# Optimization experiments

Hardware: AMD Instinct MI355X
Metric: run time of the kernel (lower is better)

## Reference

```python
import jax, jax.numpy as jnp
import numpy as np

N_NODES = 20000
N_EDGES = 240000
IN_DIM = 20
SH_DIM = 16  # (lmax+1)^2 with lmax=3
DENOM = 1.0
EPS = 1e-12


def spherical_harmonics_lmax3(v):
    """Real spherical harmonics l=0..3 on unit vectors v: [E,3] -> [E,16]."""
    x, y, z = v[:, 0], v[:, 1], v[:, 2]
    x2, y2, z2 = x * x, y * y, z * z
    sh = [
        jnp.full_like(x, 0.28209479177387814),            # l=0
        0.4886025119029199 * y,                            # l=1, m=-1
        0.4886025119029199 * z,                            # l=1, m=0
        0.4886025119029199 * x,                            # l=1, m=1
        1.0925484305920792 * x * y,                        # l=2, m=-2
        1.0925484305920792 * y * z,                        # l=2, m=-1
        0.31539156525252005 * (3.0 * z2 - 1.0),            # l=2, m=0
        1.0925484305920792 * x * z,                        # l=2, m=1
        0.5462742152960396 * (x2 - y2),                    # l=2, m=2
        0.5900435899266435 * y * (3.0 * x2 - y2),          # l=3, m=-3
        2.890611442640554 * x * y * z,                     # l=3, m=-2
        0.4570457994644658 * y * (5.0 * z2 - 1.0),         # l=3, m=-1
        0.3731763325901154 * z * (5.0 * z2 - 3.0),         # l=3, m=0
        0.4570457994644658 * x * (5.0 * z2 - 1.0),         # l=3, m=1
        1.445305721320277 * z * (x2 - y2),                 # l=3, m=2
        0.5900435899266435 * x * (x2 - 3.0 * y2),          # l=3, m=3
    ]
    return jnp.stack(sh, axis=-1)


def setup_inputs() -> dict:
    key = jax.random.key(0)
    ks = jax.random.split(key, 10)
    x = jax.random.normal(ks[0], (N_NODES, IN_DIM), dtype=jnp.float32)
    positions = jax.random.normal(ks[1], (N_NODES, 3), dtype=jnp.float32)
    edge_index = jax.random.randint(ks[2], (2, N_EDGES), 0, N_NODES, dtype=jnp.int32)
    s = 1.0 / np.sqrt(IN_DIM)
    W_pre = jax.random.uniform(ks[3], (IN_DIM, IN_DIM), jnp.float32, -s, s)
    b_pre = jax.random.uniform(ks[4], (IN_DIM,), jnp.float32, -s, s)
    W_post = jax.random.uniform(ks[5], (IN_DIM, IN_DIM), jnp.float32, -s, s)
    b_post = jax.random.uniform(ks[6], (IN_DIM,), jnp.float32, -s, s)
    W_sc = jax.random.uniform(ks[7], (IN_DIM, IN_DIM), jnp.float32, -s, s)
    b_sc = jax.random.uniform(ks[8], (IN_DIM,), jnp.float32, -s, s)
    return {"x": x, "positions": positions, "edge_index": edge_index,
            "W_pre": W_pre, "b_pre": b_pre, "W_post": W_post, "b_post": b_post,
            "W_sc": W_sc, "b_sc": b_sc}


def reference(x, positions, edge_index, W_pre, b_pre, W_post, b_post, W_sc, b_sc):
    row, col = edge_index[0], edge_index[1]
    # per-edge gather + relative positions
    rel = positions[col] - positions[row]                      # [E,3]
    norm = jnp.sqrt(jnp.sum(rel * rel, axis=-1, keepdims=True) + EPS)
    sh = spherical_harmonics_lmax3(rel / norm)                 # [E,16]
    sender = x[row]                                            # [E,20]
    # equivariant tensor product (outer product over irreps channels)
    tp = (sender[:, :, None] * sh[:, None, :]).reshape(sender.shape[0], IN_DIM * SH_DIM)  # [E,320]
    edge_features = jnp.concatenate([sender, tp], axis=1)      # [E,340]
    # scatter-add aggregation to target nodes
    aggr = jax.ops.segment_sum(edge_features, col, num_segments=N_NODES)  # [N,340]
    # node update MLP + shortcut (math of Layer.update)
    h = x / DENOM
    h = jax.nn.relu(h @ W_pre.T + b_pre)
    h = h @ W_post.T + b_post
    out = x @ W_sc.T + b_sc + h                                # [N,20]
    # aggr is computed (and aggregated) by the original propagate; concat so it stays live
    return jnp.concatenate([out, aggr], axis=1)                # [N,360]
```

## Files before the change

### kernel.cpp

```cpp
#include <hip/hip_runtime.h>
#include <stdint.h>

#define N_NODES 20000
#define N_EDGES 240000
#define IN_DIM  20
#define OUT_DIM 360
#define EPS_F   1e-12f
#define CAP     64
#define EDGE_BLOCKS ((N_EDGES + 255) / 256)
#define MLP_BLOCKS  ((N_NODES + 255) / 256)

typedef _Float16 half8   __attribute__((ext_vector_type(8)));
typedef float    floatx16 __attribute__((ext_vector_type(16)));

__device__ __forceinline__ half8 h8_from_u32(uint32_t u0, uint32_t u1,
                                             uint32_t u2, uint32_t u3) {
    union { uint32_t u[4]; half8 h; } t;
    t.u[0] = u0; t.u[1] = u1; t.u[2] = u2; t.u[3] = u3;
    return t.h;
}

__device__ __forceinline__ uint32_t maskpair(int t, int j) {
    return (t > j ? 0xFFFFu : 0u) | (t > j + 1 ? 0xFFFF0000u : 0u);
}

__device__ __forceinline__ float sh_coeff(int k, float xn, float yn, float zn) {
    const float x2 = xn * xn, y2 = yn * yn, z2 = zn * zn;
    switch (k) {
        case 0:  return 0.28209479177387814f;
        case 1:  return 0.4886025119029199f * yn;
        case 2:  return 0.4886025119029199f * zn;
        case 3:  return 0.4886025119029199f * xn;
        case 4:  return 1.0925484305920792f * xn * yn;
        case 5:  return 1.0925484305920792f * yn * zn;
        case 6:  return 0.31539156525252005f * (3.0f * z2 - 1.0f);
        case 7:  return 1.0925484305920792f * xn * zn;
        case 8:  return 0.5462742152960396f * (x2 - y2);
        case 9:  return 0.5900435899266435f * yn * (3.0f * x2 - y2);
        case 10: return 2.890611442640554f  * xn * yn * zn;
        case 11: return 0.4570457994644658f * yn * (5.0f * z2 - 1.0f);
        case 12: return 0.3731763325901154f * zn * (5.0f * z2 - 3.0f);
        case 13: return 0.4570457994644658f * xn * (5.0f * z2 - 1.0f);
        case 14: return 1.445305721320277f  * zn * (x2 - y2);
        default: return 0.5900435899266435f * xn * (x2 - 3.0f * y2);
    }
}

__global__ __launch_bounds__(256) void bucket_sh_mlp(
    const float* __restrict__ pos,
    const int* __restrict__ ei,
    const float* __restrict__ x,
    const float* __restrict__ Wpre,  const float* __restrict__ bpre,
    const float* __restrict__ Wpost, const float* __restrict__ bpost,
    const float* __restrict__ Wsc,   const float* __restrict__ bsc,
    int* __restrict__ counts,
    int* __restrict__ ovf_cnt,
    int* __restrict__ ovf,
    int* __restrict__ bucket,
    half8* __restrict__ shbuf,
    uint32_t* __restrict__ xpair,
    float* __restrict__ out)
{
    if ((int)blockIdx.x < EDGE_BLOCKS) {
        const int e = (int)(blockIdx.x * 256 + threadIdx.x);
        if (e >= N_EDGES) return;
        const int row = ei[e];
        const int col = ei[N_EDGES + e];
        const int slot = atomicAdd(&counts[col], 1);
        if (slot >= CAP) { ovf[atomicAdd(ovf_cnt, 1)] = e; return; }

        const int sidx = col * CAP + slot;
        bucket[sidx] = row;

        const float rx = pos[col * 3 + 0] - pos[row * 3 + 0];
        const float ry = pos[col * 3 + 1] - pos[row * 3 + 1];
        const float rz = pos[col * 3 + 2] - pos[row * 3 + 2];
        const float rinv = rsqrtf(rx * rx + ry * ry + rz * rz + EPS_F);
        const float xx = rx * rinv, yy = ry * rinv, zz = rz * rinv;
        const float x2 = xx * xx, y2 = yy * yy, z2 = zz * zz;

        const float sh0  = 0.28209479177387814f;
        const float sh1  = 0.4886025119029199f * yy;
        const float sh2  = 0.4886025119029199f * zz;
        const float sh3  = 0.4886025119029199f * xx;
        const float sh4  = 1.0925484305920792f * xx * yy;
        const float sh5  = 1.0925484305920792f * yy * zz;
        const float sh6  = 0.31539156525252005f * (3.0f * z2 - 1.0f);
        const float sh7  = 1.0925484305920792f * xx * zz;
        const float sh8  = 0.5462742152960396f * (x2 - y2);
        const float sh9  = 0.5900435899266435f * yy * (3.0f * x2 - y2);
        const float sh10 = 2.890611442640554f  * xx * yy * zz;
        const float sh11 = 0.4570457994644658f * yy * (5.0f * z2 - 1.0f);
        const float sh12 = 0.3731763325901154f * zz * (5.0f * z2 - 3.0f);
        const float sh13 = 0.4570457994644658f * xx * (5.0f * z2 - 1.0f);
        const float sh14 = 1.445305721320277f  * zz * (x2 - y2);
        const float sh15 = 0.5900435899266435f * xx * (x2 - 3.0f * y2);

        const half8 v0 = { (_Float16)sh0,  (_Float16)sh1,  (_Float16)sh2,  (_Float16)sh3,
                           (_Float16)sh4,  (_Float16)sh5,  (_Float16)sh6,  (_Float16)sh7 };
        const half8 v1 = { (_Float16)sh8,  (_Float16)sh9,  (_Float16)sh10, (_Float16)sh11,
                           (_Float16)sh12, (_Float16)sh13, (_Float16)sh14, (_Float16)sh15 };
        half8* dst = shbuf + (size_t)sidx * 2;
        dst[0] = v0;
        dst[1] = v1;
        return;
    }

    __shared__ float sWpre[IN_DIM * IN_DIM];
    __shared__ float sWpost[IN_DIM * IN_DIM];
    __shared__ float sWsc[IN_DIM * IN_DIM];
    __shared__ float sb[3 * IN_DIM];

    for (int t = threadIdx.x; t < IN_DIM * IN_DIM; t += 256) {
        sWpre[t]  = Wpre[t];
        sWpost[t] = Wpost[t];
        sWsc[t]   = Wsc[t];
    }
    if (threadIdx.x < IN_DIM) {
        sb[threadIdx.x]              = bpre[threadIdx.x];
        sb[IN_DIM + threadIdx.x]     = bpost[threadIdx.x];
        sb[2 * IN_DIM + threadIdx.x] = bsc[threadIdx.x];
    }
    __syncthreads();

    const int i = (int)((blockIdx.x - EDGE_BLOCKS) * 256 + threadIdx.x);
    if (i >= N_NODES) return;

    float xi[IN_DIM], h[IN_DIM];
#pragma unroll
    for (int j = 0; j < IN_DIM; ++j) xi[j] = x[(size_t)i * IN_DIM + j];

#pragma unroll
    for (int j = 0; j < IN_DIM; ++j) {
        const float v = xi[j];
        const _Float16 hh = (_Float16)v;
        const float res = v - (float)hh;
        union { _Float16 f[2]; uint32_t u; } t;
        t.f[0] = hh; t.f[1] = (_Float16)res;
        xpair[(size_t)i * IN_DIM + j] = t.u;
    }

#pragma unroll
    for (int j = 0; j < IN_DIM; ++j) {
        float a = sb[j];
#pragma unroll
        for (int kk = 0; kk < IN_DIM; ++kk) a = fmaf(xi[kk], sWpre[j * IN_DIM + kk], a);
        h[j] = fmaxf(a, 0.0f);
    }
#pragma unroll
    for (int j = 0; j < IN_DIM; ++j) {
        float a = sb[IN_DIM + j] + sb[2 * IN_DIM + j];
#pragma unroll
        for (int kk = 0; kk < IN_DIM; ++kk) {
            a = fmaf(h[kk],  sWpost[j * IN_DIM + kk], a);
            a = fmaf(xi[kk], sWsc[j * IN_DIM + kk],  a);
        }
        out[(size_t)i * OUT_DIM + j] = a;
    }
}

__global__ __launch_bounds__(256) void node_gather(
    const float* __restrict__ x,
    const float* __restrict__ pos,
    const int* __restrict__ ei,
    const int* __restrict__ counts,
    const int* __restrict__ bucket,
    const _Float16* __restrict__ shbuf,
    const uint32_t* __restrict__ xpair,
    const int* __restrict__ ovf_cnt,
    const int* __restrict__ ovf,
    float* __restrict__ out)
{
    const int lane  = threadIdx.x & 63;
    const int node  = (int)((blockIdx.x * blockDim.x + threadIdx.x) >> 6);
    const int col   = lane & 31;
    const int hi    = lane >> 5;
    const int khalf = hi * 8;
    const int rowc  = min(col, IN_DIM - 1);

    const int cnt_raw = __builtin_amdgcn_readfirstlane(counts[node]);
    const int cnt = min(cnt_raw, CAP);

    floatx16 acc = {0,0,0,0,0,0,0,0,0,0,0,0,0,0,0,0};

    if (cnt > 0) {
        const int rl = bucket[node * CAP + lane];
        const int nb = (cnt + 15) >> 4;

        for (int b = 0; b < nb; ++b) {
            const int sbase = 16 * b + khalf;

            int rr[8];
#pragma unroll
            for (int j = 0; j < 8; ++j) {
                int r = __shfl(rl, sbase + j, 64);
                rr[j] = (int)min((uint32_t)r, (uint32_t)(N_NODES - 1));
            }
            uint32_t ee[8];
#pragma unroll
            for (int j = 0; j < 8; ++j)
                ee[j] = xpair[(size_t)rr[j] * IN_DIM + rowc];

            uint32_t a1u[4], a2u[4];
#pragma unroll
            for (int p = 0; p < 4; ++p) {
                a1u[p] = (ee[2 * p] & 0xFFFFu)  | (ee[2 * p + 1] << 16);
                a2u[p] = (ee[2 * p] >> 16)      | (ee[2 * p + 1] & 0xFFFF0000u);
            }

            uint32_t B0, B1, B2, B3;
            if (col < 16) {
                const uint16_t* bp = (const uint16_t*)shbuf
                                   + (size_t)(node * CAP + sbase) * 16 + col;
                const uint32_t h0 = bp[0 * 16];
                const uint32_t h1 = bp[1 * 16];
                const uint32_t h2 = bp[2 * 16];
                const uint32_t h3 = bp[3 * 16];
                const uint32_t h4 = bp[4 * 16];
                const uint32_t h5 = bp[5 * 16];
                const uint32_t h6 = bp[6 * 16];
                const uint32_t h7 = bp[7 * 16];
                B0 = h0 | (h1 << 16);
                B1 = h2 | (h3 << 16);
                B2 = h4 | (h5 << 16);
                B3 = h6 | (h7 << 16);
            } else if (col == 16) {
                B0 = B1 = B2 = B3 = 0x3C003C00u;
            } else {
                B0 = B1 = B2 = B3 = 0u;
            }
            const int rem = cnt - 16 * b;
            if (rem < 16) {
                const int t = rem - khalf;
                B0 &= maskpair(t, 0);
                B1 &= maskpair(t, 2);
                B2 &= maskpair(t, 4);
                B3 &= maskpair(t, 6);
            }

            const half8 hb  = h8_from_u32(B0, B1, B2, B3);
            const half8 ha1 = h8_from_u32(a1u[0], a1u[1], a1u[2], a1u[3]);
            const half8 ha2 = h8_from_u32(a2u[0], a2u[1], a2u[2], a2u[3]);
            acc = __builtin_amdgcn_mfma_f32_32x32x16_f16(ha1, hb, acc, 0, 0, 0);
            acc = __builtin_amdgcn_mfma_f32_32x32x16_f16(ha2, hb, acc, 0, 0, 0);
        }
    }

    if (cnt_raw > CAP) {
        const int m = *ovf_cnt;
        for (int t2 = 0; t2 < m; ++t2) {
            const int e = ovf[t2];
            if (ei[N_EDGES + e] != node) continue;
            const int row = ei[e];
            const float rx = pos[node * 3 + 0] - pos[row * 3 + 0];
            const float ry = pos[node * 3 + 1] - pos[row * 3 + 1];
            const float rz = pos[node * 3 + 2] - pos[row * 3 + 2];
            const float rinv = rsqrtf(rx * rx + ry * ry + rz * rz + EPS_F);
            float shc;
            if (col < 16)       shc = sh_coeff(col, rx * rinv, ry * rinv, rz * rinv);
            else if (col == 16) shc = 1.0f;
            else                shc = 0.0f;
#pragma unroll
            for (int r = 0; r < 16; ++r) {
                const int rw = ((r & 3) + 8 * (r >> 2)) + 4 * hi;
                if (rw < IN_DIM)
                    acc[r] = fmaf(x[(size_t)row * IN_DIM + rw], shc, acc[r]);
            }
        }
    }

    float* orow = out + (size_t)node * OUT_DIM;
    if (col < 16) {
#pragma unroll
        for (int r = 0; r < 16; ++r) {
            const int rw = ((r & 3) + 8 * (r >> 2)) + 4 * hi;
            if (rw < IN_DIM) orow[2 * IN_DIM + rw * 16 + col] = acc[r];
        }
    } else if (col == 16) {
#pragma unroll
        for (int r = 0; r < 16; ++r) {
            const int rw = ((r & 3) + 8 * (r >> 2)) + 4 * hi;
            if (rw < IN_DIM) orow[IN_DIM + rw] = acc[r];
        }
    }
}

extern "C" void kernel_launch(void* const* d_in, const int* in_sizes, int n_in,
                              void* d_out, int out_size, void* d_ws, size_t ws_size,
                              hipStream_t stream)
{
    const float* x     = (const float*)d_in[0];
    const float* pos   = (const float*)d_in[1];
    const int*   ei    = (const int*)d_in[2];
    const float* Wpre  = (const float*)d_in[3];
    const float* bpre  = (const float*)d_in[4];
    const float* Wpost = (const float*)d_in[5];
    const float* bpost = (const float*)d_in[6];
    const float* Wsc   = (const float*)d_in[7];
    const float* bsc   = (const float*)d_in[8];
    float* out = (float*)d_out;

    half8* shbuf    = (half8*)d_ws;
    uint32_t* xpair = (uint32_t*)((char*)d_ws
                    + (size_t)N_NODES * CAP * 16 * sizeof(_Float16));
    int* ws_i    = (int*)(xpair + (size_t)N_NODES * IN_DIM);
    int* counts  = ws_i;
    int* ovf_cnt = ws_i + N_NODES;
    int* ovf     = ws_i + N_NODES + 1;
    int* bucket  = ws_i + N_NODES + 1 + N_EDGES;

    hipMemsetAsync(counts, 0, (size_t)(N_NODES + 1) * sizeof(int), stream);

    bucket_sh_mlp<<<EDGE_BLOCKS + MLP_BLOCKS, 256, 0, stream>>>(
        pos, ei, x, Wpre, bpre, Wpost, bpost, Wsc, bsc,
        counts, ovf_cnt, ovf, bucket, shbuf, xpair, out);

    node_gather<<<(N_NODES * 64) / 256, 256, 0, stream>>>(
        x, pos, ei, counts, bucket, (const _Float16*)shbuf, xpair, ovf_cnt, ovf, out);
}
```

Measured before the change: 118.6 us.

## Partition per-node edge counters across block groups with cache-line padding

Splits the single per-node atomic slot counter into eight partitions, chosen by block index, each padded to its own 64-byte line. Each partition gets a 16-slot bucket region. The gather kernel rebuilds a compact slot mapping per lane with prefix sums over the partition counts and fetches spherical-harmonic rows by shuffled slot index. The aim is to reduce atomic contention during bucketing. The cost is a much larger counter memset, a doubled sh/bucket footprint, and more scattered loads in the gather. Nodes whose partitions together exceed 64 edges without any single partition overflowing would lose edges.

```diff
diff --git a/kernel.cpp b/kernel.cpp
--- a/kernel.cpp
+++ b/kernel.cpp
@@ -6,7 +6,9 @@
 #define IN_DIM  20
 #define OUT_DIM 360
 #define EPS_F   1e-12f
-#define CAP     64
+#define NPART   8
+#define CAP_P   16
+#define SLOTS   (NPART * CAP_P)
 #define EDGE_BLOCKS ((N_EDGES + 255) / 256)
 #define MLP_BLOCKS  ((N_NODES + 255) / 256)
 
@@ -53,7 +55,7 @@
     const float* __restrict__ Wpre,  const float* __restrict__ bpre,
     const float* __restrict__ Wpost, const float* __restrict__ bpost,
     const float* __restrict__ Wsc,   const float* __restrict__ bsc,
-    int* __restrict__ counts,
+    int* __restrict__ cnt_pad,
     int* __restrict__ ovf_cnt,
     int* __restrict__ ovf,
     int* __restrict__ bucket,
@@ -64,12 +66,13 @@
     if ((int)blockIdx.x < EDGE_BLOCKS) {
         const int e = (int)(blockIdx.x * 256 + threadIdx.x);
         if (e >= N_EDGES) return;
+        const int p = (int)(blockIdx.x & (NPART - 1));
         const int row = ei[e];
         const int col = ei[N_EDGES + e];
-        const int slot = atomicAdd(&counts[col], 1);
-        if (slot >= CAP) { ovf[atomicAdd(ovf_cnt, 1)] = e; return; }
-
-        const int sidx = col * CAP + slot;
+        const int slot = atomicAdd(&cnt_pad[((size_t)(p * N_NODES + col)) << 4], 1);
+        if (slot >= CAP_P) { ovf[atomicAdd(ovf_cnt, 1)] = e; return; }
+
+        const int sidx = col * SLOTS + (p << 4) + slot;
         bucket[sidx] = row;
 
         const float rx = pos[col * 3 + 0] - pos[row * 3 + 0];
@@ -163,7 +166,7 @@
     const float* __restrict__ x,
     const float* __restrict__ pos,
     const int* __restrict__ ei,
-    const int* __restrict__ counts,
+    const int* __restrict__ cnt_pad,
     const int* __restrict__ bucket,
     const _Float16* __restrict__ shbuf,
     const uint32_t* __restrict__ xpair,
@@ -178,13 +181,34 @@
     const int khalf = hi * 8;
     const int rowc  = min(col, IN_DIM - 1);
 
-    const int cnt_raw = __builtin_amdgcn_readfirstlane(counts[node]);
-    const int cnt = min(cnt_raw, CAP);
+    int ovf_any = 0;
+    int c[NPART];
+#pragma unroll
+    for (int q = 0; q < NPART; ++q) {
+        const int cr = __builtin_amdgcn_readfirstlane(
+            cnt_pad[((size_t)(q * N_NODES + node)) << 4]);
+        ovf_any |= (cr > CAP_P);
+        c[q] = min(cr, CAP_P);
+    }
+    int pre = 0, pp = 0, base = 0;
+#pragma unroll
+    for (int q = 0; q < NPART; ++q) {
+        if (q >= 1) {
+            const int ge = (lane >= pre) ? 1 : 0;
+            pp  += ge;
+            base = ge ? pre : base;
+        }
+        pre += c[q];
+    }
+    const int cnt = min(pre, 64);
+    const int s  = min(lane - base, CAP_P - 1);
+    const int m  = (pp << 4) + s;
 
     floatx16 acc = {0,0,0,0,0,0,0,0,0,0,0,0,0,0,0,0};
 
     if (cnt > 0) {
-        const int rl = bucket[node * CAP + lane];
+        int rl = bucket[node * SLOTS + m];
+        const uint16_t* sh16 = (const uint16_t*)shbuf;
         const int nb = (cnt + 15) >> 4;
 
         for (int b = 0; b < nb; ++b) {
@@ -201,29 +225,26 @@
             for (int j = 0; j < 8; ++j)
                 ee[j] = xpair[(size_t)rr[j] * IN_DIM + rowc];
 
+            uint32_t hh[8];
+#pragma unroll
+            for (int j = 0; j < 8; ++j) {
+                const int mj = __shfl(m, sbase + j, 64);
+                hh[j] = sh16[(size_t)(node * SLOTS + mj) * 16 + (col & 15)];
+            }
+
             uint32_t a1u[4], a2u[4];
 #pragma unroll
-            for (int p = 0; p < 4; ++p) {
-                a1u[p] = (ee[2 * p] & 0xFFFFu)  | (ee[2 * p + 1] << 16);
-                a2u[p] = (ee[2 * p] >> 16)      | (ee[2 * p + 1] & 0xFFFF0000u);
+            for (int pq = 0; pq < 4; ++pq) {
+                a1u[pq] = (ee[2 * pq] & 0xFFFFu)  | (ee[2 * pq + 1] << 16);
+                a2u[pq] = (ee[2 * pq] >> 16)      | (ee[2 * pq + 1] & 0xFFFF0000u);
             }
 
             uint32_t B0, B1, B2, B3;
             if (col < 16) {
-                const uint16_t* bp = (const uint16_t*)shbuf
-                                   + (size_t)(node * CAP + sbase) * 16 + col;
-                const uint32_t h0 = bp[0 * 16];
-                const uint32_t h1 = bp[1 * 16];
-                const uint32_t h2 = bp[2 * 16];
-                const uint32_t h3 = bp[3 * 16];
-                const uint32_t h4 = bp[4 * 16];
-                const uint32_t h5 = bp[5 * 16];
-                const uint32_t h6 = bp[6 * 16];
-                const uint32_t h7 = bp[7 * 16];
-                B0 = h0 | (h1 << 16);
-                B1 = h2 | (h3 << 16);
-                B2 = h4 | (h5 << 16);
-                B3 = h6 | (h7 << 16);
+                B0 = hh[0] | (hh[1] << 16);
+                B1 = hh[2] | (hh[3] << 16);
+                B2 = hh[4] | (hh[5] << 16);
+                B3 = hh[6] | (hh[7] << 16);
             } else if (col == 16) {
                 B0 = B1 = B2 = B3 = 0x3C003C00u;
             } else {
@@ -246,9 +267,9 @@
         }
     }
 
-    if (cnt_raw > CAP) {
-        const int m = *ovf_cnt;
-        for (int t2 = 0; t2 < m; ++t2) {
+    if (ovf_any) {
+        const int mm = *ovf_cnt;
+        for (int t2 = 0; t2 < mm; ++t2) {
             const int e = ovf[t2];
             if (ei[N_EDGES + e] != node) continue;
             const int row = ei[e];
@@ -300,21 +321,20 @@
     const float* bsc   = (const float*)d_in[8];
     float* out = (float*)d_out;
 
-    half8* shbuf    = (half8*)d_ws;
-    uint32_t* xpair = (uint32_t*)((char*)d_ws
-                    + (size_t)N_NODES * CAP * 16 * sizeof(_Float16));
-    int* ws_i    = (int*)(xpair + (size_t)N_NODES * IN_DIM);
-    int* counts  = ws_i;
-    int* ovf_cnt = ws_i + N_NODES;
-    int* ovf     = ws_i + N_NODES + 1;
-    int* bucket  = ws_i + N_NODES + 1 + N_EDGES;
-
-    hipMemsetAsync(counts, 0, (size_t)(N_NODES + 1) * sizeof(int), stream);
+    char* wp = (char*)d_ws;
+    half8*    shbuf   = (half8*)wp;               wp += (size_t)N_NODES * SLOTS * 32;
+    int*      bucket  = (int*)wp;                 wp += (size_t)N_NODES * SLOTS * 4;
+    uint32_t* xpair   = (uint32_t*)wp;            wp += (size_t)N_NODES * IN_DIM * 4;
+    int*      cnt_pad = (int*)wp;                 wp += (size_t)NPART * N_NODES * 64;
+    int*      ovf_cnt = (int*)wp;                 wp += 4;
+    int*      ovf     = (int*)wp;
+
+    hipMemsetAsync(cnt_pad, 0, (size_t)NPART * N_NODES * 64 + 4, stream);
 
     bucket_sh_mlp<<<EDGE_BLOCKS + MLP_BLOCKS, 256, 0, stream>>>(
         pos, ei, x, Wpre, bpre, Wpost, bpost, Wsc, bsc,
-        counts, ovf_cnt, ovf, bucket, shbuf, xpair, out);
+        cnt_pad, ovf_cnt, ovf, bucket, shbuf, xpair, out);
 
     node_gather<<<(N_NODES * 64) / 256, 256, 0, stream>>>(
-        x, pos, ei, counts, bucket, (const _Float16*)shbuf, xpair, ovf_cnt, ovf, out);
-}
+        x, pos, ei, cnt_pad, bucket, (const _Float16*)shbuf, xpair, ovf_cnt, ovf, out);
+}
```

New measurement: 121.4 us. +2.3%, slower.
